# Kernel tuning notes

Measured on AMD Instinct MI355X. Metric: run time of the kernel, lower is better.

## Reference

```python
import jax, jax.numpy as jnp
import numpy as np

N_HEADS = 16
HEAD_DIM = 128  # d_model // n_heads


def rope(x):
    # x: [B, H, T, D]. Matches the torch module: interleaved even/odd split,
    # then concat([x1*cos - x2*sin, x1*sin + x2*cos], axis=-1).
    T, D = x.shape[2], x.shape[3]
    inv_freq = 1.0 / (10000.0 ** (jnp.arange(0, D, 2, dtype=x.dtype) / D))  # [D/2]
    freqs = jnp.arange(T, dtype=x.dtype)[:, None] * inv_freq[None, :]       # [T, D/2]
    sin, cos = jnp.sin(freqs), jnp.cos(freqs)                               # [T, D/2]
    x1, x2 = x[..., ::2], x[..., 1::2]                                      # [B,H,T,D/2]
    return jnp.concatenate([x1 * cos - x2 * sin, x1 * sin + x2 * cos], axis=-1)


def setup_inputs() -> dict:
    key = jax.random.key(0)
    ks = jax.random.split(key, 5)
    B, T, C = 2, 2048, 2048
    scale = 1.0 / np.sqrt(C)
    return {
        "x": jax.random.normal(ks[0], (B, T, C), dtype=jnp.float32),
        "W_qkv": jax.random.normal(ks[1], (3 * C, C), dtype=jnp.float32) * scale,
        "b_qkv": jnp.zeros((3 * C,), dtype=jnp.float32),
        "W_out": jax.random.normal(ks[2], (C, C), dtype=jnp.float32) * scale,
        "b_out": jnp.zeros((C,), dtype=jnp.float32),
    }


def reference(x, W_qkv, b_qkv, W_out, b_out):
    B, T, C = x.shape
    H, D = N_HEADS, HEAD_DIM
    qkv = x @ W_qkv.T + b_qkv                      # [B, T, 3C]
    qkv = qkv.reshape(B, T, 3, H, D)
    q, k, v = qkv[:, :, 0], qkv[:, :, 1], qkv[:, :, 2]  # [B, T, H, D]
    q = rope(jnp.transpose(q, (0, 2, 1, 3)))       # [B, H, T, D]
    k = rope(jnp.transpose(k, (0, 2, 1, 3)))
    v = jnp.transpose(v, (0, 2, 1, 3))
    scores = jnp.einsum("bhqd,bhkd->bhqk", q, k) / jnp.sqrt(jnp.asarray(D, x.dtype))
    causal = jnp.tril(jnp.ones((T, T), dtype=bool))
    scores = jnp.where(causal, scores, jnp.finfo(x.dtype).min)
    attn = jax.nn.softmax(scores, axis=-1)
    out = jnp.einsum("bhqk,bhkd->bhqd", attn, v)   # [B, H, T, D]
    out = jnp.transpose(out, (0, 2, 1, 3)).reshape(B, T, C)
    return out @ W_out.T + b_out
```

## Files before the change

### kernel.cpp

```cpp
#include <hip/hip_runtime.h>
#include <hip/hip_bf16.h>

typedef __attribute__((ext_vector_type(8))) short bf16x8;
typedef __attribute__((ext_vector_type(4))) float f32x4;

#define GLOAD_LDS16(gptr, lptr) \
  __builtin_amdgcn_global_load_lds((const __attribute__((address_space(1))) void*)(gptr), \
                                   (__attribute__((address_space(3))) void*)(lptr), 16, 0, 0)

__device__ __forceinline__ unsigned short f2b(float f) {
  union { float f; unsigned u; } x; x.f = f;
  unsigned r = x.u + 0x7fffu + ((x.u >> 16) & 1u);
  return (unsigned short)(r >> 16);
}
__device__ __forceinline__ float b2f(unsigned short u) {
  union { unsigned u; float f; } x; x.u = ((unsigned)u) << 16;
  return x.f;
}

__global__ void cast_kernel(const float* __restrict__ in, unsigned short* __restrict__ out, int n) {
  const int i = (blockIdx.x * 256 + threadIdx.x) * 4;
  if (i < n) {
    const float4 v = *(const float4*)(in + i);
    ushort4 r;
    r.x = f2b(v.x); r.y = f2b(v.y); r.z = f2b(v.z); r.w = f2b(v.w);
    *(ushort4*)(out + i) = r;
  }
}

template<int OUTF32>
__global__ __launch_bounds__(512, 2)
void gemm128(const unsigned short* __restrict__ A,
             const unsigned short* __restrict__ Bm,
             const float* __restrict__ bias,
             void* __restrict__ Cp,
             int M, int N, int K)
{
  __shared__ __align__(16) char Lds[98304];
  const int t  = threadIdx.x;
  const int l  = t & 63;
  const int w  = t >> 6;
  const int lr = l & 15;
  const int lkb = (l >> 4) << 4;
  const int wr = w >> 2;
  const int wc = w & 3;

  const int nwg = gridDim.x;
  const int wg  = (blockIdx.x & 7) * (nwg >> 3) + (blockIdx.x >> 3);
  const int NBN = N >> 8;
  const int bm = wg / NBN, bn = wg % NBN;

  const int sw3 = (lr & 7) << 4;
  const int ck0 = lkb ^ sw3;
  const int ck1 = (64 | lkb) ^ sw3;

  const long K2 = (long)K * 2;
  const char* Ab = (const char*)A  + (long)(bm * 128) * K2;
  const char* Bb = (const char*)Bm + (long)(bn * 256) * K2;

  auto swzsrc = [&](int lo) -> long {
    const int d = lo ^ (((lo >> 7) & 7) << 4);
    return (long)(d >> 7) * K2 + (d & 127);
  };
  const int t16 = t << 4;
  const long a0 = swzsrc(t16),          a1 = swzsrc(t16 + 8192);
  const long b0 = a0,                   b1 = a1;
  const long b2 = swzsrc(t16 + 16384),  b3 = swzsrc(t16 + 24576);

  auto stageA = [&](int g) {
    char* dst = Lds + (g & 1) * 49152 + t16;
    const char* src = Ab + (long)g * 128;
    GLOAD_LDS16(src + a0, dst);
    GLOAD_LDS16(src + a1, dst + 8192);
  };
  auto stageB2 = [&](int g, int half) {
    char* dst = Lds + (g & 1) * 49152 + 16384 + half * 16384 + t16;
    const char* src = Bb + (long)g * 128;
    GLOAD_LDS16(src + (half ? b2 : b0), dst);
    GLOAD_LDS16(src + (half ? b3 : b1), dst + 8192);
  };

  f32x4 acc[4][4] = {};
  const int NT = K >> 6;

  bf16x8 af[2][2], blo[2][2], bhi[2][2];

  stageA(0);
  stageB2(0, 0); stageB2(0, 1);
  stageB2(1, 0); stageB2(1, 1);
  asm volatile("s_waitcnt vmcnt(4)" ::: "memory");
  __builtin_amdgcn_s_barrier();
  {
    const char* AH0 = Lds + wr * 8192;
    const char* BH0 = Lds + 16384 + wc * 8192;
#pragma unroll
    for (int ni = 0; ni < 2; ++ni) {
      blo[ni][0] = *(const bf16x8*)(BH0 + ((ni * 16 + lr) << 7) + ck0);
      blo[ni][1] = *(const bf16x8*)(BH0 + ((ni * 16 + lr) << 7) + ck1);
    }
#pragma unroll
    for (int mi = 0; mi < 2; ++mi) {
      af[mi][0] = *(const bf16x8*)(AH0 + ((mi * 16 + lr) << 7) + ck0);
      af[mi][1] = *(const bf16x8*)(AH0 + ((mi * 16 + lr) << 7) + ck1);
    }
#pragma unroll
    for (int ni = 0; ni < 2; ++ni) {
      bhi[ni][0] = *(const bf16x8*)(BH0 + (((ni + 2) * 16 + lr) << 7) + ck0);
      bhi[ni][1] = *(const bf16x8*)(BH0 + (((ni + 2) * 16 + lr) << 7) + ck1);
    }
  }

  for (int tt = 0; tt < NT; ++tt) {
    const char* SB = Lds + (tt & 1) * 49152;
    const char* AH = SB + wr * 8192;

    if (tt + 1 < NT) stageA(tt + 1);
    __builtin_amdgcn_s_barrier();
    __builtin_amdgcn_sched_barrier(0);
    __builtin_amdgcn_s_setprio(1);
#pragma unroll
    for (int mi = 0; mi < 2; ++mi)
#pragma unroll
      for (int ni = 0; ni < 2; ++ni) {
        acc[mi][ni] = __builtin_amdgcn_mfma_f32_16x16x32_bf16(af[mi][0], blo[ni][0], acc[mi][ni], 0, 0, 0);
        acc[mi][ni] = __builtin_amdgcn_mfma_f32_16x16x32_bf16(af[mi][1], blo[ni][1], acc[mi][ni], 0, 0, 0);
      }
    __builtin_amdgcn_s_setprio(0);
    __builtin_amdgcn_s_barrier();
    __builtin_amdgcn_sched_barrier(0);

    __builtin_amdgcn_s_setprio(1);
#pragma unroll
    for (int mi = 0; mi < 2; ++mi)
#pragma unroll
      for (int ni = 0; ni < 2; ++ni) {
        acc[mi][ni + 2] = __builtin_amdgcn_mfma_f32_16x16x32_bf16(af[mi][0], bhi[ni][0], acc[mi][ni + 2], 0, 0, 0);
        acc[mi][ni + 2] = __builtin_amdgcn_mfma_f32_16x16x32_bf16(af[mi][1], bhi[ni][1], acc[mi][ni + 2], 0, 0, 0);
      }
    __builtin_amdgcn_s_setprio(0);
#pragma unroll
    for (int mi = 0; mi < 2; ++mi) {
      af[mi][0] = *(const bf16x8*)(AH + (((mi + 2) * 16 + lr) << 7) + ck0);
      af[mi][1] = *(const bf16x8*)(AH + (((mi + 2) * 16 + lr) << 7) + ck1);
    }
    __builtin_amdgcn_s_barrier();
    __builtin_amdgcn_sched_barrier(0);

    asm volatile("s_waitcnt vmcnt(0)" ::: "memory");
    if (tt + 2 < NT) stageB2(tt + 2, 0);
    __builtin_amdgcn_s_setprio(1);
#pragma unroll
    for (int mi = 0; mi < 2; ++mi)
#pragma unroll
      for (int ni = 0; ni < 2; ++ni) {
        acc[mi + 2][ni] = __builtin_amdgcn_mfma_f32_16x16x32_bf16(af[mi][0], blo[ni][0], acc[mi + 2][ni], 0, 0, 0);
        acc[mi + 2][ni] = __builtin_amdgcn_mfma_f32_16x16x32_bf16(af[mi][1], blo[ni][1], acc[mi + 2][ni], 0, 0, 0);
      }
    __builtin_amdgcn_s_setprio(0);
    if (tt + 1 < NT) {
      const char* BHn = Lds + ((tt + 1) & 1) * 49152 + 16384 + wc * 8192;
#pragma unroll
      for (int ni = 0; ni < 2; ++ni) {
        blo[ni][0] = *(const bf16x8*)(BHn + ((ni * 16 + lr) << 7) + ck0);
        blo[ni][1] = *(const bf16x8*)(BHn + ((ni * 16 + lr) << 7) + ck1);
      }
    }
    __builtin_amdgcn_s_barrier();
    __builtin_amdgcn_sched_barrier(0);

    if (tt + 2 < NT) stageB2(tt + 2, 1);
    __builtin_amdgcn_s_setprio(1);
#pragma unroll
    for (int mi = 0; mi < 2; ++mi)
#pragma unroll
      for (int ni = 0; ni < 2; ++ni) {
        acc[mi + 2][ni + 2] = __builtin_amdgcn_mfma_f32_16x16x32_bf16(af[mi][0], bhi[ni][0], acc[mi + 2][ni + 2], 0, 0, 0);
        acc[mi + 2][ni + 2] = __builtin_amdgcn_mfma_f32_16x16x32_bf16(af[mi][1], bhi[ni][1], acc[mi + 2][ni + 2], 0, 0, 0);
      }
    __builtin_amdgcn_s_setprio(0);
    if (tt + 1 < NT) {
      const char* SBn = Lds + ((tt + 1) & 1) * 49152;
      const char* AHn = SBn + wr * 8192;
      const char* BHn = SBn + 16384 + wc * 8192;
#pragma unroll
      for (int mi = 0; mi < 2; ++mi) {
        af[mi][0] = *(const bf16x8*)(AHn + ((mi * 16 + lr) << 7) + ck0);
        af[mi][1] = *(const bf16x8*)(AHn + ((mi * 16 + lr) << 7) + ck1);
      }
#pragma unroll
      for (int ni = 0; ni < 2; ++ni) {
        bhi[ni][0] = *(const bf16x8*)(BHn + (((ni + 2) * 16 + lr) << 7) + ck0);
        bhi[ni][1] = *(const bf16x8*)(BHn + (((ni + 2) * 16 + lr) << 7) + ck1);
      }
    }
    __builtin_amdgcn_s_barrier();
    __builtin_amdgcn_sched_barrier(0);
  }

  const int roff = (l >> 4) << 2;
  const int row0 = bm * 128 + wr * 64 + roff;
  const int col0 = bn * 256 + wc * 64 + lr;
  float bv[4];
#pragma unroll
  for (int ni = 0; ni < 4; ++ni) bv[ni] = bias ? bias[col0 + ni * 16] : 0.0f;
#pragma unroll
  for (int mi = 0; mi < 4; ++mi) {
#pragma unroll
    for (int r = 0; r < 4; ++r) {
      const long rb = (long)(row0 + mi * 16 + r) * N;
#pragma unroll
      for (int ni = 0; ni < 4; ++ni) {
        const float v = acc[mi][ni][r] + bv[ni];
        if (OUTF32) ((float*)Cp)[rb + col0 + ni * 16] = v;
        else ((unsigned short*)Cp)[rb + col0 + ni * 16] = f2b(v);
      }
    }
  }
}

__global__ void prep_kernel(const unsigned short* __restrict__ qkv,
                            unsigned short* __restrict__ Qr,
                            unsigned short* __restrict__ Kr,
                            unsigned short* __restrict__ Vt)
{
  const int T = 2048;
  __shared__ unsigned short ld[128][65];
  const int bh = blockIdx.y, tb = blockIdx.x;
  const int b = bh >> 4, h = bh & 15;
  const int t = threadIdx.x;

#pragma unroll
  for (int i = 0; i < 16; ++i) {
    const int idx = i * 256 + t;
    const int d  = idx & 63;
    const int tt = tb * 64 + (idx >> 6);
    const long base = ((long)(b * T + tt) * 3) * 2048 + h * 128;
    const float inv = exp2f(-(float)d * 0.2076205059304602f);
    const float fr = (float)tt * inv;
    float sn, cs;
    sincosf(fr, &sn, &cs);
    const float q1 = b2f(qkv[base + 2 * d]);
    const float q2 = b2f(qkv[base + 2 * d + 1]);
    const float k1 = b2f(qkv[base + 2048 + 2 * d]);
    const float k2 = b2f(qkv[base + 2048 + 2 * d + 1]);
    const long ob = ((long)bh * T + tt) * 128;
    Qr[ob + d]      = f2b(q1 * cs - q2 * sn);
    Qr[ob + 64 + d] = f2b(q1 * sn + q2 * cs);
    Kr[ob + d]      = f2b(k1 * cs - k2 * sn);
    Kr[ob + 64 + d] = f2b(k1 * sn + k2 * cs);
  }

#pragma unroll
  for (int i = 0; i < 32; ++i) {
    const int idx = i * 256 + t;
    const int d = idx & 127, tr = idx >> 7;
    ld[d][tr] = qkv[((long)(b * T + tb * 64 + tr) * 3 + 2) * 2048 + h * 128 + d];
  }
  __syncthreads();
#pragma unroll
  for (int i = 0; i < 32; ++i) {
    const int idx = i * 256 + t;
    const int tc = idx & 63, dr = idx >> 6;
    Vt[((long)bh * 128 + dr) * T + tb * 64 + tc] = ld[dr][tc];
  }
}

__global__ __launch_bounds__(256)
void attn_fwd(const unsigned short* __restrict__ Q,
              const unsigned short* __restrict__ Kg,
              const unsigned short* __restrict__ Vt,
              unsigned short* __restrict__ O, int T)
{
  __shared__ __align__(16) unsigned short Ks[2][64 * 128];
  __shared__ __align__(16) unsigned short Vs[2][128 * 64];
  __shared__ __align__(16) unsigned short Ps[4][16 * 64];
  const int t = threadIdx.x;
  const int w = t >> 6, l = t & 63;
  const int lr = l & 15;
  const int g16 = (l >> 4) << 4;
  const int sw = (lr & 7) << 4;
  const int bh = blockIdx.x;
  const int qt = (gridDim.y - 1) - blockIdx.y;
  const int q0 = qt * 64 + w * 16;
  const long hbase = (long)bh * T * 128;
  const long hbase2 = hbase * 2;
  const long T2 = (long)T * 2;
  const int roff = (l >> 4) << 2;
  const float C1 = 0.08838834764831845f * 1.4426950408889634f;

  bf16x8 qf[4];
  const unsigned short* Qrow = Q + hbase + (long)(q0 + lr) * 128;
#pragma unroll
  for (int ds = 0; ds < 4; ++ds) qf[ds] = *(const bf16x8*)&Qrow[ds * 32 + (g16 >> 1)];

  f32x4 o[8] = {};
  float m[4]    = {-INFINITY, -INFINITY, -INFINITY, -INFINITY};
  float lsum[4] = {0.f, 0.f, 0.f, 0.f};

  auto stage = [&](int kt, int buf) {
#pragma unroll
    for (int c = 0; c < 4; ++c) {
      const int o2 = t * 16 + c * 4096;
      const int krow = o2 >> 8, kcb = o2 & 255;
      GLOAD_LDS16((const char*)Kg + hbase2 + (long)kt * 16384 + krow * 256 + (kcb ^ ((krow & 7) << 4)),
                  (char*)Ks[buf] + o2);
      const int vrow = o2 >> 7, vcb = o2 & 127;
      GLOAD_LDS16((const char*)Vt + (long)(bh * 128 + vrow) * T2 + (long)kt * 128 + (vcb ^ ((vrow & 7) << 4)),
                  (char*)Vs[buf] + o2);
    }
  };

  const int ntile = qt + 1;
  stage(0, 0);
  __syncthreads();

  for (int kt = 0; kt < ntile; ++kt) {
    const int cur = kt & 1;
    if (kt + 1 < ntile) stage(kt + 1, cur ^ 1);

    const char* KsB = (const char*)Ks[cur];
    const char* VsB = (const char*)Vs[cur];

    f32x4 s[4] = {};
    __builtin_amdgcn_s_setprio(1);
#pragma unroll
    for (int tj = 0; tj < 4; ++tj)
#pragma unroll
      for (int ds = 0; ds < 4; ++ds) {
        bf16x8 kf = *(const bf16x8*)(KsB + (tj * 16 + lr) * 256 + ((ds * 64 + g16) ^ sw));
        s[tj] = __builtin_amdgcn_mfma_f32_16x16x32_bf16(qf[ds], kf, s[tj], 0, 0, 0);
      }
    __builtin_amdgcn_s_setprio(0);

    if (kt == qt) {
#pragma unroll
      for (int tj = 0; tj < 4; ++tj)
#pragma unroll
        for (int j = 0; j < 4; ++j)
          if (kt * 64 + tj * 16 + lr > q0 + roff + j) s[tj][j] = -INFINITY;
    }

    float corr[4];
#pragma unroll
    for (int j = 0; j < 4; ++j) {
      float v = fmaxf(fmaxf(s[0][j], s[1][j]), fmaxf(s[2][j], s[3][j]));
      v = fmaxf(v, __shfl_xor(v, 1, 64));
      v = fmaxf(v, __shfl_xor(v, 2, 64));
      v = fmaxf(v, __shfl_xor(v, 4, 64));
      v = fmaxf(v, __shfl_xor(v, 8, 64));
      const float mn = fmaxf(m[j], v * C1);
      corr[j] = exp2f(m[j] - mn);
      m[j] = mn;
    }
    float rs[4] = {0.f, 0.f, 0.f, 0.f};
#pragma unroll
    for (int tj = 0; tj < 4; ++tj)
#pragma unroll
      for (int j = 0; j < 4; ++j) {
        const float p = exp2f(fmaf(s[tj][j], C1, -m[j]));
        rs[j] += p;
        const int prow = roff + j;
        *(unsigned short*)((char*)Ps[w] + prow * 128 + (((tj * 16 + lr) * 2) ^ ((prow & 7) << 4))) = f2b(p);
      }
#pragma unroll
    for (int j = 0; j < 4; ++j) {
      float v = rs[j];
      v += __shfl_xor(v, 1, 64);
      v += __shfl_xor(v, 2, 64);
      v += __shfl_xor(v, 4, 64);
      v += __shfl_xor(v, 8, 64);
      lsum[j] = lsum[j] * corr[j] + v;
    }
#pragma unroll
    for (int nj = 0; nj < 8; ++nj)
#pragma unroll
      for (int j = 0; j < 4; ++j) o[nj][j] *= corr[j];

    __builtin_amdgcn_s_setprio(1);
#pragma unroll
    for (int ks = 0; ks < 2; ++ks) {
      bf16x8 pf = *(const bf16x8*)((const char*)Ps[w] + lr * 128 + ((ks * 64 + g16) ^ sw));
#pragma unroll
      for (int nj = 0; nj < 8; ++nj) {
        bf16x8 vf = *(const bf16x8*)(VsB + (nj * 16 + lr) * 128 + ((ks * 64 + g16) ^ sw));
        o[nj] = __builtin_amdgcn_mfma_f32_16x16x32_bf16(pf, vf, o[nj], 0, 0, 0);
      }
    }
    __builtin_amdgcn_s_setprio(0);
    __syncthreads();
  }

  float inv[4];
#pragma unroll
  for (int j = 0; j < 4; ++j) inv[j] = 1.0f / lsum[j];
  const int b = bh >> 4, h = bh & 15;
#pragma unroll
  for (int nj = 0; nj < 8; ++nj)
#pragma unroll
    for (int j = 0; j < 4; ++j) {
      const int q = q0 + roff + j;
      const int d = nj * 16 + lr;
      O[(long)(b * T + q) * 2048 + h * 128 + d] = f2b(o[nj][j] * inv[j]);
    }
}

extern "C" void kernel_launch(void* const* d_in, const int* in_sizes, int n_in,
                              void* d_out, int out_size, void* d_ws, size_t ws_size,
                              hipStream_t stream)
{
  const int B = 2, T = 2048, C = 2048;
  const int M = B * T;
  const int N1 = 3 * C;
  const float* x    = (const float*)d_in[0];
  const float* Wqkv = (const float*)d_in[1];
  const float* bqkv = (const float*)d_in[2];
  const float* Wout = (const float*)d_in[3];
  const float* bout = (const float*)d_in[4];
  float* out = (float*)d_out;

  char* p = (char*)d_ws;
  unsigned short* xb    = (unsigned short*)p; p += (size_t)M * C * 2;
  unsigned short* wqkvb = (unsigned short*)p; p += (size_t)N1 * C * 2;
  unsigned short* woutb = (unsigned short*)p; p += (size_t)C * C * 2;
  unsigned short* qkv   = (unsigned short*)p; p += (size_t)M * N1 * 2;
  unsigned short* Qr    = (unsigned short*)p; p += (size_t)M * C * 2;
  unsigned short* Kr    = (unsigned short*)p; p += (size_t)M * C * 2;
  unsigned short* Vt    = (unsigned short*)p; p += (size_t)M * C * 2;
  unsigned short* Ob    = xb;

  cast_kernel<<<M * C / 1024, 256, 0, stream>>>(x, xb, M * C);
  cast_kernel<<<N1 * C / 1024, 256, 0, stream>>>(Wqkv, wqkvb, N1 * C);
  cast_kernel<<<C * C / 1024, 256, 0, stream>>>(Wout, woutb, C * C);

  gemm128<0><<<dim3((M / 128) * (N1 / 256)), 512, 0, stream>>>(xb, wqkvb, bqkv, qkv, M, N1, C);

  prep_kernel<<<dim3(T / 64, 32), 256, 0, stream>>>(qkv, Qr, Kr, Vt);

  attn_fwd<<<dim3(32, T / 64), 256, 0, stream>>>(Qr, Kr, Vt, Ob, T);

  gemm128<1><<<dim3((M / 128) * (C / 256)), 512, 0, stream>>>(Ob, woutb, bout, out, M, C, C);
}
```

Measured before the change: 310.2 us.

## Restructure GEMM mainloop to triple-buffered K=32 stages for higher occupancy

Replaces the double-buffered K=64 mainloop, which had split A/B staging and four barrier phases, with a triple-buffered ring of K=32 tiles. Each stage is issued as three 16-byte global-to-LDS loads and needs only one waitcnt/barrier per iteration. LDS usage drops from 96KB to 72KB and launch bounds request 4 blocks per SM instead of 2, aiming for more waves to hide latency. The trade-off is twice as many iterations, each with a single barrier and 16 MFMAs, so per-tile overlap of LDS reads with compute is coarser. Also, 4 blocks of 72KB will not fit in LDS, so actual occupancy may stay limited.

```diff
diff --git a/kernel.cpp b/kernel.cpp
--- a/kernel.cpp
+++ b/kernel.cpp
@@ -29,14 +29,14 @@
 }
 
 template<int OUTF32>
-__global__ __launch_bounds__(512, 2)
+__global__ __launch_bounds__(512, 4)
 void gemm128(const unsigned short* __restrict__ A,
              const unsigned short* __restrict__ Bm,
              const float* __restrict__ bias,
              void* __restrict__ Cp,
              int M, int N, int K)
 {
-  __shared__ __align__(16) char Lds[98304];
+  __shared__ __align__(16) char Lds[73728];
   const int t  = threadIdx.x;
   const int l  = t & 63;
   const int w  = t >> 6;
@@ -50,151 +50,73 @@
   const int NBN = N >> 8;
   const int bm = wg / NBN, bn = wg % NBN;
 
-  const int sw3 = (lr & 7) << 4;
-  const int ck0 = lkb ^ sw3;
-  const int ck1 = (64 | lkb) ^ sw3;
-
   const long K2 = (long)K * 2;
   const char* Ab = (const char*)A  + (long)(bm * 128) * K2;
   const char* Bb = (const char*)Bm + (long)(bn * 256) * K2;
 
-  auto swzsrc = [&](int lo) -> long {
-    const int d = lo ^ (((lo >> 7) & 7) << 4);
-    return (long)(d >> 7) * K2 + (d & 127);
+  auto swz = [](int a) -> int { return a ^ (((a >> 7) & 3) << 4); };
+
+  const int t16 = t << 4;
+  const int da  = swz(t16);
+  const long sa = (long)(da >> 6) * K2 + (da & 63);
+  const int db0 = swz(t16), db1 = swz(8192 + t16);
+  const long sb0 = (long)(db0 >> 6) * K2 + (db0 & 63);
+  const long sb1 = (long)(db1 >> 6) * K2 + (db1 & 63);
+
+  auto stage = [&](int g) {
+    char* S = Lds + (g % 3) * 24576;
+    const char* As = Ab + (long)g * 64;
+    const char* Bs = Bb + (long)g * 64;
+    GLOAD_LDS16(As + sa,  S + t16);
+    GLOAD_LDS16(Bs + sb0, S + 8192 + t16);
+    GLOAD_LDS16(Bs + sb1, S + 16384 + t16);
   };
-  const int t16 = t << 4;
-  const long a0 = swzsrc(t16),          a1 = swzsrc(t16 + 8192);
-  const long b0 = a0,                   b1 = a1;
-  const long b2 = swzsrc(t16 + 16384),  b3 = swzsrc(t16 + 24576);
-
-  auto stageA = [&](int g) {
-    char* dst = Lds + (g & 1) * 49152 + t16;
-    const char* src = Ab + (long)g * 128;
-    GLOAD_LDS16(src + a0, dst);
-    GLOAD_LDS16(src + a1, dst + 8192);
-  };
-  auto stageB2 = [&](int g, int half) {
-    char* dst = Lds + (g & 1) * 49152 + 16384 + half * 16384 + t16;
-    const char* src = Bb + (long)g * 128;
-    GLOAD_LDS16(src + (half ? b2 : b0), dst);
-    GLOAD_LDS16(src + (half ? b3 : b1), dst + 8192);
-  };
+
+  int aoff[4], boff[4];
+#pragma unroll
+  for (int mi = 0; mi < 4; ++mi) {
+    const int a = ((wr * 64 + mi * 16 + lr) << 6) | lkb;
+    aoff[mi] = swz(a);
+  }
+#pragma unroll
+  for (int ni = 0; ni < 4; ++ni) {
+    const int a = ((wc * 64 + ni * 16 + lr) << 6) | lkb;
+    boff[ni] = 8192 + swz(a);
+  }
 
   f32x4 acc[4][4] = {};
-  const int NT = K >> 6;
-
-  bf16x8 af[2][2], blo[2][2], bhi[2][2];
-
-  stageA(0);
-  stageB2(0, 0); stageB2(0, 1);
-  stageB2(1, 0); stageB2(1, 1);
-  asm volatile("s_waitcnt vmcnt(4)" ::: "memory");
+  const int NT = K >> 5;
+  bf16x8 af[4], bfr[4];
+
+  stage(0); stage(1);
+  asm volatile("s_waitcnt vmcnt(3)" ::: "memory");
   __builtin_amdgcn_s_barrier();
-  {
-    const char* AH0 = Lds + wr * 8192;
-    const char* BH0 = Lds + 16384 + wc * 8192;
-#pragma unroll
-    for (int ni = 0; ni < 2; ++ni) {
-      blo[ni][0] = *(const bf16x8*)(BH0 + ((ni * 16 + lr) << 7) + ck0);
-      blo[ni][1] = *(const bf16x8*)(BH0 + ((ni * 16 + lr) << 7) + ck1);
-    }
-#pragma unroll
-    for (int mi = 0; mi < 2; ++mi) {
-      af[mi][0] = *(const bf16x8*)(AH0 + ((mi * 16 + lr) << 7) + ck0);
-      af[mi][1] = *(const bf16x8*)(AH0 + ((mi * 16 + lr) << 7) + ck1);
-    }
-#pragma unroll
-    for (int ni = 0; ni < 2; ++ni) {
-      bhi[ni][0] = *(const bf16x8*)(BH0 + (((ni + 2) * 16 + lr) << 7) + ck0);
-      bhi[ni][1] = *(const bf16x8*)(BH0 + (((ni + 2) * 16 + lr) << 7) + ck1);
-    }
-  }
+  __builtin_amdgcn_sched_barrier(0);
+#pragma unroll
+  for (int mi = 0; mi < 4; ++mi) af[mi]  = *(const bf16x8*)(Lds + aoff[mi]);
+#pragma unroll
+  for (int ni = 0; ni < 4; ++ni) bfr[ni] = *(const bf16x8*)(Lds + boff[ni]);
 
   for (int tt = 0; tt < NT; ++tt) {
-    const char* SB = Lds + (tt & 1) * 49152;
-    const char* AH = SB + wr * 8192;
-
-    if (tt + 1 < NT) stageA(tt + 1);
-    __builtin_amdgcn_s_barrier();
-    __builtin_amdgcn_sched_barrier(0);
+    if (tt + 2 < NT) stage(tt + 2);
     __builtin_amdgcn_s_setprio(1);
 #pragma unroll
-    for (int mi = 0; mi < 2; ++mi)
-#pragma unroll
-      for (int ni = 0; ni < 2; ++ni) {
-        acc[mi][ni] = __builtin_amdgcn_mfma_f32_16x16x32_bf16(af[mi][0], blo[ni][0], acc[mi][ni], 0, 0, 0);
-        acc[mi][ni] = __builtin_amdgcn_mfma_f32_16x16x32_bf16(af[mi][1], blo[ni][1], acc[mi][ni], 0, 0, 0);
-      }
-    __builtin_amdgcn_s_setprio(0);
-    __builtin_amdgcn_s_barrier();
-    __builtin_amdgcn_sched_barrier(0);
-
-    __builtin_amdgcn_s_setprio(1);
-#pragma unroll
-    for (int mi = 0; mi < 2; ++mi)
-#pragma unroll
-      for (int ni = 0; ni < 2; ++ni) {
-        acc[mi][ni + 2] = __builtin_amdgcn_mfma_f32_16x16x32_bf16(af[mi][0], bhi[ni][0], acc[mi][ni + 2], 0, 0, 0);
-        acc[mi][ni + 2] = __builtin_amdgcn_mfma_f32_16x16x32_bf16(af[mi][1], bhi[ni][1], acc[mi][ni + 2], 0, 0, 0);
-      }
-    __builtin_amdgcn_s_setprio(0);
-#pragma unroll
-    for (int mi = 0; mi < 2; ++mi) {
-      af[mi][0] = *(const bf16x8*)(AH + (((mi + 2) * 16 + lr) << 7) + ck0);
-      af[mi][1] = *(const bf16x8*)(AH + (((mi + 2) * 16 + lr) << 7) + ck1);
-    }
-    __builtin_amdgcn_s_barrier();
-    __builtin_amdgcn_sched_barrier(0);
-
-    asm volatile("s_waitcnt vmcnt(0)" ::: "memory");
-    if (tt + 2 < NT) stageB2(tt + 2, 0);
-    __builtin_amdgcn_s_setprio(1);
-#pragma unroll
-    for (int mi = 0; mi < 2; ++mi)
-#pragma unroll
-      for (int ni = 0; ni < 2; ++ni) {
-        acc[mi + 2][ni] = __builtin_amdgcn_mfma_f32_16x16x32_bf16(af[mi][0], blo[ni][0], acc[mi + 2][ni], 0, 0, 0);
-        acc[mi + 2][ni] = __builtin_amdgcn_mfma_f32_16x16x32_bf16(af[mi][1], blo[ni][1], acc[mi + 2][ni], 0, 0, 0);
-      }
+    for (int mi = 0; mi < 4; ++mi)
+#pragma unroll
+      for (int ni = 0; ni < 4; ++ni)
+        acc[mi][ni] = __builtin_amdgcn_mfma_f32_16x16x32_bf16(af[mi], bfr[ni], acc[mi][ni], 0, 0, 0);
     __builtin_amdgcn_s_setprio(0);
     if (tt + 1 < NT) {
-      const char* BHn = Lds + ((tt + 1) & 1) * 49152 + 16384 + wc * 8192;
-#pragma unroll
-      for (int ni = 0; ni < 2; ++ni) {
-        blo[ni][0] = *(const bf16x8*)(BHn + ((ni * 16 + lr) << 7) + ck0);
-        blo[ni][1] = *(const bf16x8*)(BHn + ((ni * 16 + lr) << 7) + ck1);
-      }
-    }
-    __builtin_amdgcn_s_barrier();
-    __builtin_amdgcn_sched_barrier(0);
-
-    if (tt + 2 < NT) stageB2(tt + 2, 1);
-    __builtin_amdgcn_s_setprio(1);
-#pragma unroll
-    for (int mi = 0; mi < 2; ++mi)
-#pragma unroll
-      for (int ni = 0; ni < 2; ++ni) {
-        acc[mi + 2][ni + 2] = __builtin_amdgcn_mfma_f32_16x16x32_bf16(af[mi][0], bhi[ni][0], acc[mi + 2][ni + 2], 0, 0, 0);
-        acc[mi + 2][ni + 2] = __builtin_amdgcn_mfma_f32_16x16x32_bf16(af[mi][1], bhi[ni][1], acc[mi + 2][ni + 2], 0, 0, 0);
-      }
-    __builtin_amdgcn_s_setprio(0);
-    if (tt + 1 < NT) {
-      const char* SBn = Lds + ((tt + 1) & 1) * 49152;
-      const char* AHn = SBn + wr * 8192;
-      const char* BHn = SBn + 16384 + wc * 8192;
-#pragma unroll
-      for (int mi = 0; mi < 2; ++mi) {
-        af[mi][0] = *(const bf16x8*)(AHn + ((mi * 16 + lr) << 7) + ck0);
-        af[mi][1] = *(const bf16x8*)(AHn + ((mi * 16 + lr) << 7) + ck1);
-      }
-#pragma unroll
-      for (int ni = 0; ni < 2; ++ni) {
-        bhi[ni][0] = *(const bf16x8*)(BHn + (((ni + 2) * 16 + lr) << 7) + ck0);
-        bhi[ni][1] = *(const bf16x8*)(BHn + (((ni + 2) * 16 + lr) << 7) + ck1);
-      }
-    }
-    __builtin_amdgcn_s_barrier();
-    __builtin_amdgcn_sched_barrier(0);
+      if (tt + 2 < NT) asm volatile("s_waitcnt vmcnt(3)" ::: "memory");
+      else             asm volatile("s_waitcnt vmcnt(0)" ::: "memory");
+      __builtin_amdgcn_s_barrier();
+      __builtin_amdgcn_sched_barrier(0);
+      const char* S = Lds + ((tt + 1) % 3) * 24576;
+#pragma unroll
+      for (int mi = 0; mi < 4; ++mi) af[mi]  = *(const bf16x8*)(S + aoff[mi]);
+#pragma unroll
+      for (int ni = 0; ni < 4; ++ni) bfr[ni] = *(const bf16x8*)(S + boff[ni]);
+    }
   }
 
   const int roff = (l >> 4) << 2;
```

New measurement: 307.5 us. About the same (-0.9%).
